# Performance work log

Hardware: AMD Instinct MI355X
Metric: run time of the kernel (lower is better)

## Reference

```python
import jax, jax.numpy as jnp
import numpy as np

B, S, E, H, D, NE, R = 2, 2048, 2048, 16, 128, 8, 16
HALF = D // 2
THETA = 10000.0


def setup_inputs() -> dict:
    key = jax.random.key(0)
    ks = jax.random.split(key, 18)

    def w(k, shape, fan_in):
        return jax.random.normal(k, shape, jnp.float32) / np.float32(np.sqrt(fan_in))

    inp = {
        "x": jax.random.normal(ks[0], (B, S, E), jnp.float32),
        "expert_mask": jax.random.uniform(ks[1], (B, S, NE), dtype=jnp.float32),
    }
    for i, n in enumerate(("q", "k", "v")):
        inp["W" + n] = w(ks[2 + 3 * i], (H * D, E), E)
        inp["b" + n] = jnp.zeros((H * D,), jnp.float32)
        inp["A" + n] = w(ks[3 + 3 * i], (NE, R, E), E)
        inp["B" + n] = w(ks[4 + 3 * i], (H * D, NE, R), R)
    inp["Wo"] = w(ks[11], (E, H * D), H * D)
    inp["bo"] = jnp.zeros((E,), jnp.float32)
    inp["Ao"] = w(ks[12], (NE, R, H * D), H * D)
    inp["Bo"] = w(ks[13], (E, NE, R), R)
    return inp


def routed_linear(x, W, b, A, Bm, mask):
    """MaybeRoutedLinear: dense base + expert-routed low-rank path gated by mask [B,S,NE]."""
    y = jnp.einsum("bsi,oi->bso", x, W) + b
    h = jnp.einsum("bsi,eri->bser", x, A) * mask[..., None]  # [B,S,NE,R]
    return y + jnp.einsum("bser,oer->bso", h, Bm)


def apply_rope(t):
    """Llama-style rotary embedding. t: [B,S,H,D]."""
    inv_freq = 1.0 / (THETA ** (jnp.arange(0, D, 2, dtype=jnp.float32) / D))  # [D/2]
    freqs = jnp.arange(S, dtype=jnp.float32)[:, None] * inv_freq[None, :]  # [S,D/2]
    cos = jnp.concatenate([jnp.cos(freqs)] * 2, -1)[None, :, None, :]  # [1,S,1,D]
    sin = jnp.concatenate([jnp.sin(freqs)] * 2, -1)[None, :, None, :]
    rot = jnp.concatenate([-t[..., HALF:], t[..., :HALF]], -1)
    return t * cos + rot * sin


def reference(x, expert_mask, Wq, bq, Aq, Bq, Wk, bk, Ak, Bk, Wv, bv, Av, Bv, Wo, bo, Ao, Bo):
    q = routed_linear(x, Wq, bq, Aq, Bq, expert_mask).reshape(B, S, H, D)
    k = routed_linear(x, Wk, bk, Ak, Bk, expert_mask).reshape(B, S, H, D)
    v = routed_linear(x, Wv, bv, Av, Bv, expert_mask).reshape(B, S, H, D)
    q = apply_rope(q)
    k = apply_rope(k)
    scores = jnp.einsum("bqhd,bkhd->bhqk", q, k) / jnp.float32(np.sqrt(D))
    causal = jnp.tril(jnp.ones((S, S), dtype=bool))
    scores = jnp.where(causal[None, None], scores, jnp.finfo(scores.dtype).min)
    probs = jax.nn.softmax(scores, axis=-1)
    o = jnp.einsum("bhqk,bkhd->bqhd", probs, v).reshape(B, S, H * D)
    return routed_linear(o, Wo, bo, Ao, Bo, expert_mask)
```

## Files before the change

### kernel.cpp

```cpp
#include <hip/hip_runtime.h>


#define B_ 2
#define S_ 2048
#define E_ 2048
#define H_ 16
#define D_ 128
#define NE_ 8
#define R_ 16
#define HD_ 2048
#define M_ 4096
#define KL_ 128

typedef unsigned short u16;
typedef unsigned int u32;
typedef __attribute__((ext_vector_type(8))) short bf16x8;
typedef __attribute__((ext_vector_type(4))) float f32x4;

typedef const __attribute__((address_space(1))) void gvoid_t;
typedef __attribute__((address_space(3))) void svoid_t;

__device__ __forceinline__ float bf2f(u16 u) {
    union { u32 i; float f; } v; v.i = ((u32)u) << 16; return v.f;
}
__device__ __forceinline__ u16 f2bf(float f) {
    union { float f; u32 i; } v; v.f = f;
    u32 x = v.i;
    return (u16)((x + 0x7fffu + ((x >> 16) & 1u)) >> 16);
}
__device__ __forceinline__ float ldf(const void* p, size_t i, int f) {
    return f ? ((const float*)p)[i] : bf2f(((const u16*)p)[i]);
}
__device__ __forceinline__ float4 ld4(const void* p, size_t i, int f) {
    if (f) return *(const float4*)((const float*)p + i);
    ushort4 v = *(const ushort4*)((const u16*)p + i);
    return make_float4(bf2f(v.x), bf2f(v.y), bf2f(v.z), bf2f(v.w));
}

__global__ void k_detect(const void* __restrict__ x, int* __restrict__ flags) {
    __shared__ int votes[2];
    int tid = threadIdx.x;
    if (tid < 2) votes[tid] = 0;
    __syncthreads();
    const u32* p = (const u32*)x;
    int bad = 0, tot = 0;
    for (int i = tid; i < 4096; i += 64) {
        u32 lo = p[i] & 0xffffu;
        if (lo) {
            tot++;
            int e = (int)((lo >> 7) & 0xffu);
            if (e < 100 || e > 150) bad++;
        }
    }
    atomicAdd(&votes[0], bad);
    atomicAdd(&votes[1], tot);
    __syncthreads();
    if (tid == 0) flags[0] = (votes[1] > 0 && votes[0] * 10 > votes[1] * 3) ? 1 : 0;
}

__global__ void k_cvt(const void* __restrict__ src, u16* __restrict__ dst, int n,
                      const int* __restrict__ flags) {
    int fin = flags[0];
    int i = (blockIdx.x * 256 + threadIdx.x) * 4;
    if (i >= n) return;
    float4 v = ld4(src, i, fin);
    ushort4 o;
    o.x = f2bf(v.x); o.y = f2bf(v.y); o.z = f2bf(v.z); o.w = f2bf(v.w);
    *(ushort4*)(dst + i) = o;
}

#define NX_  8388608L
#define NA1_ 262144L
#define NW_  4194304L
__global__ void k_cvt_all(
    const void* __restrict__ x,
    const void* __restrict__ Aq, const void* __restrict__ Ak,
    const void* __restrict__ Av, const void* __restrict__ Ao,
    const void* __restrict__ Bq, const void* __restrict__ Bk,
    const void* __restrict__ Bv, const void* __restrict__ Bo,
    const void* __restrict__ Wq, const void* __restrict__ Wk,
    const void* __restrict__ Wv,
    u16* __restrict__ Xb, u16* __restrict__ Acat, u16* __restrict__ Bmcat,
    u16* __restrict__ Wcat,
    const int* __restrict__ flags) {
    int fin = flags[0];
    long i = (long)(blockIdx.x * 256 + threadIdx.x) * 4;
    const void* src; u16* dst; long off;
    if (i < NX_) { src = x; dst = Xb; off = i; }
    else if (i < NX_ + 4 * NA1_) {
        long j = i - NX_; int p = (int)(j >> 18); off = j & (NA1_ - 1);
        src = (p == 0) ? Aq : (p == 1) ? Ak : (p == 2) ? Av : Ao;
        dst = Acat + (long)p * NA1_;
    } else if (i < NX_ + 8 * NA1_) {
        long j = i - NX_ - 4 * NA1_; int p = (int)(j >> 18); off = j & (NA1_ - 1);
        src = (p == 0) ? Bq : (p == 1) ? Bk : (p == 2) ? Bv : Bo;
        dst = Bmcat + (long)p * NA1_;
    } else {
        long j = i - NX_ - 8 * NA1_; int p = (int)(j / NW_); off = j - (long)p * NW_;
        src = (p == 0) ? Wq : (p == 1) ? Wk : Wv;
        dst = Wcat + (long)p * NW_;
    }
    float4 v = ld4(src, off, fin);
    ushort4 o;
    o.x = f2bf(v.x); o.y = f2bf(v.y); o.z = f2bf(v.z); o.w = f2bf(v.w);
    *(ushort4*)(dst + off) = o;
}

#define BM_ 128
#define BN_ 128
#define BK_ 64

__global__ __launch_bounds__(256, 2) void k_gemm_mfma(
    const u16* __restrict__ A, int lda,
    const u16* __restrict__ Bw, int ldb, int K1,
    const u16* __restrict__ A2, int lda2,
    const u16* __restrict__ B2, int K2,
    const void* __restrict__ bias, const void* __restrict__ mask,
    void* __restrict__ C, int ldc, int store_mode,
    const int* __restrict__ flags) {
    __shared__ __align__(16) u16 As[BM_ * BK_];
    __shared__ __align__(16) u16 Bs[BN_ * BK_];
    int fin = flags[0];
    int tid = threadIdx.x;
    int w = tid >> 6, lane = tid & 63;
    int l15 = lane & 15, quad = lane >> 4;
    int wm = w >> 1, wn = w & 1;
    int m0 = blockIdx.y * BM_, n0 = blockIdx.x * BN_;
    int lrow = lane >> 3;
    int lcol = (lane & 7) * 8;

    f32x4 acc[4][4];
#pragma unroll
    for (int mt = 0; mt < 4; mt++)
#pragma unroll
        for (int nt = 0; nt < 4; nt++)
#pragma unroll
            for (int r = 0; r < 4; r++) acc[mt][nt][r] = 0.f;

    int n1 = K1 / BK_, n2 = K2 / BK_;
    int total = n1 + n2;
    for (int it = 0; it < total; it++) {
        const u16 *pa, *pb; int sa, sb, kb;
        if (it < n1) { pa = A;  sa = lda;  pb = Bw; sb = ldb; kb = it * BK_; }
        else         { pa = A2; sa = lda2; pb = B2; sb = K2;  kb = (it - n1) * BK_; }
        __syncthreads();
#pragma unroll
        for (int i = 0; i < 4; i++) {
            int rowb = (w * 4 + i) * 8;
            int r = rowb + lrow;
            __builtin_amdgcn_global_load_lds(
                (gvoid_t*)(pa + (size_t)(m0 + r) * sa + kb + lcol),
                (svoid_t*)(As + rowb * BK_), 16, 0, 0);
            __builtin_amdgcn_global_load_lds(
                (gvoid_t*)(pb + (size_t)(n0 + r) * sb + kb + lcol),
                (svoid_t*)(Bs + rowb * BK_), 16, 0, 0);
        }
        __syncthreads();
#pragma unroll
        for (int kk = 0; kk < 2; kk++) {
            int ko = kk * 32 + quad * 8;
            bf16x8 af[4], bf[4];
#pragma unroll
            for (int mt = 0; mt < 4; mt++)
                af[mt] = *(const bf16x8*)(As + (wm * 64 + mt * 16 + l15) * BK_ + ko);
#pragma unroll
            for (int nt = 0; nt < 4; nt++)
                bf[nt] = *(const bf16x8*)(Bs + (wn * 64 + nt * 16 + l15) * BK_ + ko);
#pragma unroll
            for (int mt = 0; mt < 4; mt++)
#pragma unroll
                for (int nt = 0; nt < 4; nt++)
                    acc[mt][nt] = __builtin_amdgcn_mfma_f32_16x16x32_bf16(
                        af[mt], bf[nt], acc[mt][nt], 0, 0, 0);
        }
    }

#pragma unroll
    for (int mt = 0; mt < 4; mt++) {
#pragma unroll
        for (int r = 0; r < 4; r++) {
            int m = m0 + wm * 64 + mt * 16 + quad * 4 + r;
#pragma unroll
            for (int nt = 0; nt < 4; nt++) {
                int n = n0 + wn * 64 + nt * 16 + l15;
                float v = acc[mt][nt][r];
                if (bias) v += ldf(bias, (size_t)n, fin);
                if (mask) v *= ldf(mask, (size_t)m * NE_ + ((n & 127) >> 4), fin);
                int f32out = (store_mode == 2) ? fin : store_mode;
                if (f32out) ((float*)C)[(size_t)m * ldc + n] = v;
                else        ((u16*)C)[(size_t)m * ldc + n] = f2bf(v);
            }
        }
    }
}

#define GBM 256
#define GBN 256
#define GBK 32

__global__ __launch_bounds__(512, 2) void k_gemm256(
    const u16* __restrict__ A, int lda,
    const u16* __restrict__ Bw, int ldb, int K1,
    const u16* __restrict__ A2, int lda2,
    const u16* __restrict__ B2, int K2,
    const void* __restrict__ bias0, const void* __restrict__ bias1,
    const void* __restrict__ bias2,
    void* __restrict__ C, int ldc, int store_mode,
    const int* __restrict__ flags) {
    __shared__ __align__(16) u16 As[4][GBM * GBK];
    __shared__ __align__(16) u16 Bs[4][GBN * GBK];
    int fin = flags[0];
    int tid = threadIdx.x;
    int w = tid >> 6, lane = tid & 63;
    int l15 = lane & 15, quad = lane >> 4;
    int wm = w >> 2, wn = w & 3;

    int nxt = gridDim.x;
    int lin = blockIdx.y * gridDim.x + blockIdx.x;
    int cpx = (gridDim.x * gridDim.y) >> 3;
    int wg = (lin & 7) * cpx + (lin >> 3);
    int m0 = (wg / nxt) * GBM;
    int n0 = (wg % nxt) * GBN;

    int p = (store_mode == 3) ? (n0 >> 11) : 0;
    const u16* A2p = A2 + p * 128;
    const u16* B2p = B2 + (long)p * NA1_;
    int nloc = (store_mode == 3) ? (n0 & 2047) : n0;

    int srow = tid >> 2;
    int scol = (tid & 3) * 8;
    int nk1 = K1 >> 5;
    int NT = nk1 + (K2 >> 5);

    f32x4 acc[8][4];
#pragma unroll
    for (int mt = 0; mt < 8; mt++)
#pragma unroll
        for (int nt = 0; nt < 4; nt++)
#pragma unroll
            for (int r = 0; r < 4; r++) acc[mt][nt][r] = 0.f;

    auto stage = [&](int kt) {
        const u16 *pa, *pb; int sa, sb, kb, nb;
        if (kt < nk1) { pa = A;   sa = lda;  pb = Bw;  sb = ldb; kb = kt * GBK; nb = n0; }
        else          { pa = A2p; sa = lda2; pb = B2p; sb = K2;  kb = (kt - nk1) * GBK; nb = nloc; }
        int buf = kt & 3;
#pragma unroll
        for (int j = 0; j < 2; j++) {
            __builtin_amdgcn_global_load_lds(
                (gvoid_t*)(pa + (size_t)(m0 + j * 128 + srow) * sa + kb + scol),
                (svoid_t*)(&As[buf][(j * 128 + w * 16) * GBK]), 16, 0, 0);
            __builtin_amdgcn_global_load_lds(
                (gvoid_t*)(pb + (size_t)(nb + j * 128 + srow) * sb + kb + scol),
                (svoid_t*)(&Bs[buf][(j * 128 + w * 16) * GBK]), 16, 0, 0);
        }
    };

    stage(0);
    if (NT > 1) stage(1);
    if (NT > 2) stage(2);

    for (int kt = 0; kt < NT; kt++) {
        int buf = kt & 3;
        if (kt + 3 < NT) {
            stage(kt + 3);
            asm volatile("s_waitcnt vmcnt(12)" ::: "memory");
        } else {
            int rem = NT - 1 - kt;
            if (rem >= 2)      asm volatile("s_waitcnt vmcnt(8)" ::: "memory");
            else if (rem == 1) asm volatile("s_waitcnt vmcnt(4)" ::: "memory");
            else               asm volatile("s_waitcnt vmcnt(0)" ::: "memory");
        }
        __builtin_amdgcn_s_barrier();
        __builtin_amdgcn_sched_barrier(0);

        bf16x8 af[8], bfr[4];
#pragma unroll
        for (int mt = 0; mt < 8; mt++)
            af[mt] = *(const bf16x8*)(&As[buf][(wm * 128 + mt * 16 + l15) * GBK + quad * 8]);
#pragma unroll
        for (int nt = 0; nt < 4; nt++)
            bfr[nt] = *(const bf16x8*)(&Bs[buf][(wn * 64 + nt * 16 + l15) * GBK + quad * 8]);

        __builtin_amdgcn_s_setprio(1);
#pragma unroll
        for (int mt = 0; mt < 8; mt++)
#pragma unroll
            for (int nt = 0; nt < 4; nt++)
                acc[mt][nt] = __builtin_amdgcn_mfma_f32_16x16x32_bf16(
                    af[mt], bfr[nt], acc[mt][nt], 0, 0, 0);
        __builtin_amdgcn_s_setprio(0);

        __builtin_amdgcn_s_barrier();
        __builtin_amdgcn_sched_barrier(0);
    }

    const void* bp = (store_mode == 3) ? (p == 0 ? bias0 : p == 1 ? bias1 : bias2)
                                       : bias0;
#pragma unroll
    for (int mt = 0; mt < 8; mt++) {
#pragma unroll
        for (int r = 0; r < 4; r++) {
            int m = m0 + wm * 128 + mt * 16 + quad * 4 + r;
#pragma unroll
            for (int nt = 0; nt < 4; nt++) {
                int n = n0 + wn * 64 + nt * 16 + l15;
                float v = acc[mt][nt][r];
                if (bp) v += ldf(bp, (size_t)(n & 2047), fin);
                if (store_mode == 3) {
                    ((u16*)C)[(size_t)p * 8388608 + (size_t)m * 2048 + (n & 2047)] = f2bf(v);
                } else {
                    if (fin) ((float*)C)[(size_t)m * ldc + n] = v;
                    else     ((u16*)C)[(size_t)m * ldc + n] = f2bf(v);
                }
            }
        }
    }
}

__global__ void k_rope2(u16* __restrict__ Q, u16* __restrict__ K) {
    const int n = M_ * HD_ / 2;
    int idx = blockIdx.x * 256 + threadIdx.x;
    u16* Y = (idx < n) ? Q : K;
    int id = (idx < n) ? idx : idx - n;
    int d2 = id & 63;
    int sh = id >> 6;
    int s = (sh >> 4) & (S_ - 1);
    float inv = powf(10000.f, -(float)d2 * (1.f / 64.f));
    float fr = (float)s * inv;
    float c, sn;
    sincosf(fr, &sn, &c);
    size_t base = ((size_t)sh) << 7;
    float t0 = bf2f(Y[base + d2]);
    float t1 = bf2f(Y[base + d2 + 64]);
    Y[base + d2]      = f2bf(t0 * c - t1 * sn);
    Y[base + d2 + 64] = f2bf(t1 * c + t0 * sn);
}

__global__ void k_transpose_v(const u16* __restrict__ Vb, u16* __restrict__ Vt) {
    __shared__ u16 t[32][33];
    int s0 = blockIdx.x * 32;
    int n0 = blockIdx.y * 32;
    int b  = blockIdx.z;
    int tx = threadIdx.x & 31, ty = threadIdx.x >> 5;
#pragma unroll
    for (int r = 0; r < 4; r++)
        t[ty + r * 8][tx] = Vb[((size_t)(b * S_ + s0 + ty + r * 8)) * HD_ + n0 + tx];
    __syncthreads();
#pragma unroll
    for (int r = 0; r < 4; r++)
        Vt[((size_t)(b * HD_ + n0 + ty + r * 8)) * S_ + s0 + tx] = t[tx][ty + r * 8];
}

#define KS_ST 136
#define VT_ST 72
#define SCALE_ 0.088388347648318447f

__global__ __launch_bounds__(256, 3) void k_flash6(
    const u16* __restrict__ Q, const u16* __restrict__ K,
    const u16* __restrict__ Vt, u16* __restrict__ O) {
    __shared__ __align__(16) u16 Ks[64 * KS_ST];
    __shared__ __align__(16) u16 Vs[128 * VT_ST];
    __shared__ __align__(16) u16 Ps[64 * VT_ST];
    int tid = threadIdx.x;
    int w = tid >> 6, lane = tid & 63;
    int l15 = lane & 15, quad = lane >> 4;
    int bh = blockIdx.y, b = bh >> 4, h = bh & 15;
    int t = 31 - blockIdx.x;
    int q0 = t * 64;

    int krow[4], kd8[4], vd[4], vkg[4];
#pragma unroll
    for (int it = 0; it < 4; it++) {
        int idx = it * 256 + tid;
        krow[it] = idx >> 4; kd8[it] = (idx & 15) * 8;
        vd[it] = idx >> 3;   vkg[it] = (idx & 7) * 8;
    }

    bf16x8 qf[4];
    size_t baseQ = ((size_t)(b * S_ + q0 + w * 16 + l15)) * HD_ + h * D_;
#pragma unroll
    for (int ks = 0; ks < 4; ks++)
        qf[ks] = *(const bf16x8*)(Q + baseQ + ks * 32 + quad * 8);

    f32x4 of[8];
#pragma unroll
    for (int nt = 0; nt < 8; nt++)
#pragma unroll
        for (int r = 0; r < 4; r++) of[nt][r] = 0.f;
    float mreg = -30000.f, lreg = 0.f;
    int qrow = q0 + w * 16 + l15;

    int nch = t + 1;

    bf16x8 kpre[4], vpre[4];
#pragma unroll
    for (int it = 0; it < 4; it++) {
        kpre[it] = *(const bf16x8*)(K + ((size_t)(b * S_ + krow[it])) * HD_ + h * D_ + kd8[it]);
        vpre[it] = *(const bf16x8*)(Vt + ((size_t)(bh * 128 + vd[it])) * S_ + vkg[it]);
    }

    for (int c = 0; c < nch; c++) {
        int k0 = c * 64;
        __syncthreads();
#pragma unroll
        for (int it = 0; it < 4; it++) {
            *(bf16x8*)(Ks + krow[it] * KS_ST + kd8[it]) = kpre[it];
            *(bf16x8*)(Vs + vd[it] * VT_ST + vkg[it]) = vpre[it];
        }
        __syncthreads();
        if (c + 1 < nch) {
            int k1 = k0 + 64;
#pragma unroll
            for (int it = 0; it < 4; it++) {
                kpre[it] = *(const bf16x8*)(K + ((size_t)(b * S_ + k1 + krow[it])) * HD_ + h * D_ + kd8[it]);
                vpre[it] = *(const bf16x8*)(Vt + ((size_t)(bh * 128 + vd[it])) * S_ + k1 + vkg[it]);
            }
        }

        f32x4 sf[4];
#pragma unroll
        for (int nt = 0; nt < 4; nt++)
#pragma unroll
            for (int r = 0; r < 4; r++) sf[nt][r] = 0.f;
#pragma unroll
        for (int ks = 0; ks < 4; ks++) {
            int koff = ks * 32 + quad * 8;
            bf16x8 qa = qf[ks];
#pragma unroll
            for (int nt = 0; nt < 4; nt++) {
                bf16x8 kb = *(const bf16x8*)(Ks + (nt * 16 + l15) * KS_ST + koff);
                sf[nt] = __builtin_amdgcn_mfma_f32_16x16x32_bf16(kb, qa, sf[nt], 0, 0, 0);
            }
        }

#pragma unroll
        for (int nt = 0; nt < 4; nt++) {
            int keyb = k0 + nt * 16 + quad * 4;
#pragma unroll
            for (int r = 0; r < 4; r++) {
                float sv = sf[nt][r] * SCALE_;
                sf[nt][r] = (keyb + r > qrow) ? -30000.f : sv;
            }
        }

        float t0 = fmaxf(fmaxf(sf[0][0], sf[0][1]), fmaxf(sf[0][2], sf[0][3]));
        float t1 = fmaxf(fmaxf(sf[1][0], sf[1][1]), fmaxf(sf[1][2], sf[1][3]));
        float t2 = fmaxf(fmaxf(sf[2][0], sf[2][1]), fmaxf(sf[2][2], sf[2][3]));
        float t3 = fmaxf(fmaxf(sf[3][0], sf[3][1]), fmaxf(sf[3][2], sf[3][3]));
        float cmax = fmaxf(fmaxf(t0, t1), fmaxf(t2, t3));
        cmax = fmaxf(cmax, __shfl_xor(cmax, 16, 64));
        cmax = fmaxf(cmax, __shfl_xor(cmax, 32, 64));
        float mnew = fmaxf(mreg, cmax);
        float a = __expf(mreg - mnew);
        mreg = mnew;
#pragma unroll
        for (int nt = 0; nt < 4; nt++)
#pragma unroll
            for (int r = 0; r < 4; r++)
                sf[nt][r] = __expf(sf[nt][r] - mnew);
        float s0 = (sf[0][0] + sf[0][1]) + (sf[0][2] + sf[0][3]);
        float s1 = (sf[1][0] + sf[1][1]) + (sf[1][2] + sf[1][3]);
        float s2 = (sf[2][0] + sf[2][1]) + (sf[2][2] + sf[2][3]);
        float s3 = (sf[3][0] + sf[3][1]) + (sf[3][2] + sf[3][3]);
        float psum = (s0 + s1) + (s2 + s3);
        psum += __shfl_xor(psum, 16, 64);
        psum += __shfl_xor(psum, 32, 64);
        lreg = lreg * a + psum;

        float al[4];
#pragma unroll
        for (int r = 0; r < 4; r++) al[r] = __shfl(a, quad * 4 + r, 16);

#pragma unroll
        for (int nt = 0; nt < 4; nt++)
#pragma unroll
            for (int r = 0; r < 4; r++)
                Ps[(w * 16 + l15) * VT_ST + nt * 16 + quad * 4 + r] = f2bf(sf[nt][r]);
#pragma unroll
        for (int nt = 0; nt < 8; nt++)
#pragma unroll
            for (int r = 0; r < 4; r++) of[nt][r] *= al[r];

#pragma unroll
        for (int ks2 = 0; ks2 < 2; ks2++) {
            int koff = ks2 * 32 + quad * 8;
            bf16x8 pa = *(const bf16x8*)(Ps + (w * 16 + l15) * VT_ST + koff);
#pragma unroll
            for (int nt = 0; nt < 8; nt++) {
                bf16x8 vb = *(const bf16x8*)(Vs + (nt * 16 + l15) * VT_ST + koff);
                of[nt] = __builtin_amdgcn_mfma_f32_16x16x32_bf16(pa, vb, of[nt], 0, 0, 0);
            }
        }
    }

    float linv = 1.f / lreg;
    float inv[4];
#pragma unroll
    for (int r = 0; r < 4; r++) inv[r] = __shfl(linv, quad * 4 + r, 16);
    int rowb = q0 + w * 16 + quad * 4;
#pragma unroll
    for (int r = 0; r < 4; r++) {
        size_t base = ((size_t)(b * S_ + rowb + r)) * HD_ + h * D_;
#pragma unroll
        for (int nt = 0; nt < 8; nt++)
            O[base + nt * 16 + l15] = f2bf(of[nt][r] * inv[r]);
    }
}

extern "C" void kernel_launch(void* const* d_in, const int* in_sizes, int n_in,
                              void* d_out, int out_size, void* d_ws, size_t ws_size,
                              hipStream_t stream) {
    const void* x    = d_in[0];
    const void* mask = d_in[1];
    const void* Wq = d_in[2];  const void* bq = d_in[3];
    const void* Aq = d_in[4];  const void* Bq = d_in[5];
    const void* Wk = d_in[6];  const void* bk = d_in[7];
    const void* Ak = d_in[8];  const void* Bk = d_in[9];
    const void* Wv = d_in[10]; const void* bv = d_in[11];
    const void* Av = d_in[12]; const void* Bv = d_in[13];
    const void* Wo = d_in[14]; const void* bo = d_in[15];
    const void* Ao = d_in[16]; const void* Bo = d_in[17];

    char* ws = (char*)d_ws;
    const long MB = 1 << 20;
    int* flags = (int*)ws;
    u16* Xb    = (u16*)(ws + 1  * MB);
    u16* Acat  = (u16*)(ws + 17 * MB);
    u16* Bmcat = (u16*)(ws + 19 * MB);
    u16* hg3   = (u16*)(ws + 21 * MB);
    u16* hgo   = (u16*)(ws + 24 * MB);
    u16* Qb    = (u16*)(ws + 25 * MB);
    u16* Kb    = (u16*)(ws + 41 * MB);
    u16* Vb    = (u16*)(ws + 57 * MB);
    u16* Vt    = (u16*)(ws + 73 * MB);
    u16* Wcat  = (u16*)(ws + 73 * MB);
    u16* Wob   = Qb;
    u16* Ob    = Vb;

    k_detect<<<1, 64, 0, stream>>>(x, flags);
    const long NCVT = NX_ + 8 * NA1_ + 3 * NW_;
    k_cvt_all<<<NCVT / 1024, 256, 0, stream>>>(
        x, Aq, Ak, Av, Ao, Bq, Bk, Bv, Bo, Wq, Wk, Wv,
        Xb, Acat, Bmcat, Wcat, flags);

    k_gemm_mfma<<<dim3(3, M_ / BM_), 256, 0, stream>>>(
        Xb, E_, Acat, E_, E_, nullptr, 0, nullptr, 0,
        nullptr, mask, hg3, 384, 0, flags);

    k_gemm256<<<dim3(6144 / GBN, M_ / GBM), 512, 0, stream>>>(
        Xb, E_, Wcat, E_, E_, hg3, 384, Bmcat, KL_,
        bq, bk, bv, Qb, HD_, 3, flags);

    k_rope2<<<(M_ * HD_) / 256, 256, 0, stream>>>(Qb, Kb);
    k_transpose_v<<<dim3(S_ / 32, HD_ / 32, B_), 256, 0, stream>>>(Vb, Vt);

    k_flash6<<<dim3(32, 32), 256, 0, stream>>>(Qb, Kb, Vt, Ob);

    k_cvt<<<NW_ / 1024, 256, 0, stream>>>(Wo, Wob, (int)NW_, flags);
    k_gemm_mfma<<<dim3(1, M_ / BM_), 256, 0, stream>>>(
        Ob, HD_, Acat + 3 * NA1_, E_, E_, nullptr, 0, nullptr, 0,
        nullptr, mask, hgo, KL_, 0, flags);
    k_gemm256<<<dim3(HD_ / GBN, M_ / GBM), 512, 0, stream>>>(
        Ob, HD_, Wob, E_, E_, hgo, KL_, Bmcat + 3 * NA1_, KL_,
        bo, nullptr, nullptr, d_out, HD_, 2, flags);
}
```

Before: 798.5 us.

## Split-K low-rank projection GEMMs and retile main GEMMs with double buffering

The skinny low-rank down-projection GEMMs become split-K kernels across four K slices. They accumulate into zeroed fp32 buffers with atomics, and a separate pass converts the result to bf16, so the small grids fill more of the GPU. The large GEMM becomes a template over N tile width: 256 for the QKV projection and 128 for the output projection, which gives the output GEMM more blocks. It also drops from 4-stage to 2-stage LDS buffering and uses a fragment-major LDS layout. The cost is extra zero and convert launches, atomic traffic, and less prefetch depth, which may expose memory latency.

```diff
diff --git a/kernel.cpp b/kernel.cpp
--- a/kernel.cpp
+++ b/kernel.cpp
@@ -67,6 +67,20 @@
     ushort4 o;
     o.x = f2bf(v.x); o.y = f2bf(v.y); o.z = f2bf(v.z); o.w = f2bf(v.w);
     *(ushort4*)(dst + i) = o;
+}
+
+__global__ void k_cvtf(const float* __restrict__ src, u16* __restrict__ dst, int n) {
+    int i = (blockIdx.x * 256 + threadIdx.x) * 4;
+    if (i >= n) return;
+    float4 v = *(const float4*)(src + i);
+    ushort4 o;
+    o.x = f2bf(v.x); o.y = f2bf(v.y); o.z = f2bf(v.z); o.w = f2bf(v.w);
+    *(ushort4*)(dst + i) = o;
+}
+
+__global__ void k_zero(float4* __restrict__ p, int n4) {
+    int i = blockIdx.x * 256 + threadIdx.x;
+    if (i < n4) p[i] = make_float4(0.f, 0.f, 0.f, 0.f);
 }
 
 #define NX_  8388608L
@@ -110,13 +124,11 @@
 #define BN_ 128
 #define BK_ 64
 
-__global__ __launch_bounds__(256, 2) void k_gemm_mfma(
+__global__ __launch_bounds__(256, 2) void k_gemm_sk(
     const u16* __restrict__ A, int lda,
-    const u16* __restrict__ Bw, int ldb, int K1,
-    const u16* __restrict__ A2, int lda2,
-    const u16* __restrict__ B2, int K2,
-    const void* __restrict__ bias, const void* __restrict__ mask,
-    void* __restrict__ C, int ldc, int store_mode,
+    const u16* __restrict__ Bw, int ldb, int K,
+    const void* __restrict__ mask,
+    float* __restrict__ Cf, int ldc,
     const int* __restrict__ flags) {
     __shared__ __align__(16) u16 As[BM_ * BK_];
     __shared__ __align__(16) u16 Bs[BN_ * BK_];
@@ -137,22 +149,20 @@
 #pragma unroll
             for (int r = 0; r < 4; r++) acc[mt][nt][r] = 0.f;
 
-    int n1 = K1 / BK_, n2 = K2 / BK_;
-    int total = n1 + n2;
-    for (int it = 0; it < total; it++) {
-        const u16 *pa, *pb; int sa, sb, kb;
-        if (it < n1) { pa = A;  sa = lda;  pb = Bw; sb = ldb; kb = it * BK_; }
-        else         { pa = A2; sa = lda2; pb = B2; sb = K2;  kb = (it - n1) * BK_; }
+    int iters = (K / BK_) / gridDim.z;
+    int it0 = blockIdx.z * iters;
+    for (int it = it0; it < it0 + iters; it++) {
+        int kb = it * BK_;
         __syncthreads();
 #pragma unroll
         for (int i = 0; i < 4; i++) {
             int rowb = (w * 4 + i) * 8;
             int r = rowb + lrow;
             __builtin_amdgcn_global_load_lds(
-                (gvoid_t*)(pa + (size_t)(m0 + r) * sa + kb + lcol),
+                (gvoid_t*)(A + (size_t)(m0 + r) * lda + kb + lcol),
                 (svoid_t*)(As + rowb * BK_), 16, 0, 0);
             __builtin_amdgcn_global_load_lds(
-                (gvoid_t*)(pb + (size_t)(n0 + r) * sb + kb + lcol),
+                (gvoid_t*)(Bw + (size_t)(n0 + r) * ldb + kb + lcol),
                 (svoid_t*)(Bs + rowb * BK_), 16, 0, 0);
         }
         __syncthreads();
@@ -183,21 +193,14 @@
 #pragma unroll
             for (int nt = 0; nt < 4; nt++) {
                 int n = n0 + wn * 64 + nt * 16 + l15;
-                float v = acc[mt][nt][r];
-                if (bias) v += ldf(bias, (size_t)n, fin);
-                if (mask) v *= ldf(mask, (size_t)m * NE_ + ((n & 127) >> 4), fin);
-                int f32out = (store_mode == 2) ? fin : store_mode;
-                if (f32out) ((float*)C)[(size_t)m * ldc + n] = v;
-                else        ((u16*)C)[(size_t)m * ldc + n] = f2bf(v);
-            }
-        }
-    }
-}
-
-#define GBM 256
-#define GBN 256
-#define GBK 32
-
+                float v = acc[mt][nt][r] * ldf(mask, (size_t)m * NE_ + ((n & 127) >> 4), fin);
+                atomicAdd(&Cf[(size_t)m * ldc + n], v);
+            }
+        }
+    }
+}
+
+template <int BNt>
 __global__ __launch_bounds__(512, 2) void k_gemm256(
     const u16* __restrict__ A, int lda,
     const u16* __restrict__ Bw, int ldb, int K1,
@@ -207,86 +210,90 @@
     const void* __restrict__ bias2,
     void* __restrict__ C, int ldc, int store_mode,
     const int* __restrict__ flags) {
-    __shared__ __align__(16) u16 As[4][GBM * GBK];
-    __shared__ __align__(16) u16 Bs[4][GBN * GBK];
+    constexpr int NTF = BNt / 64;
+    __shared__ __align__(16) u16 As[2][256 * 32];
+    __shared__ __align__(16) u16 Bs[2][BNt * 32];
     int fin = flags[0];
     int tid = threadIdx.x;
     int w = tid >> 6, lane = tid & 63;
     int l15 = lane & 15, quad = lane >> 4;
     int wm = w >> 2, wn = w & 3;
 
-    int nxt = gridDim.x;
     int lin = blockIdx.y * gridDim.x + blockIdx.x;
     int cpx = (gridDim.x * gridDim.y) >> 3;
     int wg = (lin & 7) * cpx + (lin >> 3);
-    int m0 = (wg / nxt) * GBM;
-    int n0 = (wg % nxt) * GBN;
+    int m0 = (wg / gridDim.x) * 256;
+    int n0 = (wg % gridDim.x) * BNt;
 
     int p = (store_mode == 3) ? (n0 >> 11) : 0;
     const u16* A2p = A2 + p * 128;
     const u16* B2p = B2 + (long)p * NA1_;
     int nloc = (store_mode == 3) ? (n0 & 2047) : n0;
 
-    int srow = tid >> 2;
-    int scol = (tid & 3) * 8;
     int nk1 = K1 >> 5;
     int NT = nk1 + (K2 >> 5);
 
-    f32x4 acc[8][4];
+    f32x4 acc[8][NTF];
 #pragma unroll
     for (int mt = 0; mt < 8; mt++)
 #pragma unroll
-        for (int nt = 0; nt < 4; nt++)
+        for (int nt = 0; nt < NTF; nt++)
 #pragma unroll
             for (int r = 0; r < 4; r++) acc[mt][nt][r] = 0.f;
 
     auto stage = [&](int kt) {
-        const u16 *pa, *pb; int sa, sb, kb, nb;
-        if (kt < nk1) { pa = A;   sa = lda;  pb = Bw;  sb = ldb; kb = kt * GBK; nb = n0; }
-        else          { pa = A2p; sa = lda2; pb = B2p; sb = K2;  kb = (kt - nk1) * GBK; nb = nloc; }
-        int buf = kt & 3;
+        const u16 *pa, *pb; size_t sa, sb; int kb, nb;
+        if (kt < nk1) { pa = A;   sa = lda;  pb = Bw;  sb = ldb; kb = kt * 32; nb = n0; }
+        else          { pa = A2p; sa = lda2; pb = B2p; sb = K2;  kb = (kt - nk1) * 32; nb = nloc; }
+        int buf = kt & 1;
 #pragma unroll
         for (int j = 0; j < 2; j++) {
+            int s = w * 2 + j;
             __builtin_amdgcn_global_load_lds(
-                (gvoid_t*)(pa + (size_t)(m0 + j * 128 + srow) * sa + kb + scol),
-                (svoid_t*)(&As[buf][(j * 128 + w * 16) * GBK]), 16, 0, 0);
+                (gvoid_t*)(pa + (size_t)(m0 + s * 16 + l15) * sa + kb + quad * 8),
+                (svoid_t*)(&As[buf][s * 512]), 16, 0, 0);
+        }
+        if constexpr (BNt == 256) {
+#pragma unroll
+            for (int j = 0; j < 2; j++) {
+                int s = w * 2 + j;
+                __builtin_amdgcn_global_load_lds(
+                    (gvoid_t*)(pb + (size_t)(nb + s * 16 + l15) * sb + kb + quad * 8),
+                    (svoid_t*)(&Bs[buf][s * 512]), 16, 0, 0);
+            }
+        } else {
             __builtin_amdgcn_global_load_lds(
-                (gvoid_t*)(pb + (size_t)(nb + j * 128 + srow) * sb + kb + scol),
-                (svoid_t*)(&Bs[buf][(j * 128 + w * 16) * GBK]), 16, 0, 0);
+                (gvoid_t*)(pb + (size_t)(nb + w * 16 + l15) * sb + kb + quad * 8),
+                (svoid_t*)(&Bs[buf][w * 512]), 16, 0, 0);
         }
     };
 
     stage(0);
-    if (NT > 1) stage(1);
-    if (NT > 2) stage(2);
-
     for (int kt = 0; kt < NT; kt++) {
-        int buf = kt & 3;
-        if (kt + 3 < NT) {
-            stage(kt + 3);
-            asm volatile("s_waitcnt vmcnt(12)" ::: "memory");
+        int buf = kt & 1;
+        if (kt + 1 < NT) {
+            stage(kt + 1);
+            if constexpr (BNt == 256) asm volatile("s_waitcnt vmcnt(4)" ::: "memory");
+            else                      asm volatile("s_waitcnt vmcnt(3)" ::: "memory");
         } else {
-            int rem = NT - 1 - kt;
-            if (rem >= 2)      asm volatile("s_waitcnt vmcnt(8)" ::: "memory");
-            else if (rem == 1) asm volatile("s_waitcnt vmcnt(4)" ::: "memory");
-            else               asm volatile("s_waitcnt vmcnt(0)" ::: "memory");
+            asm volatile("s_waitcnt vmcnt(0)" ::: "memory");
         }
         __builtin_amdgcn_s_barrier();
         __builtin_amdgcn_sched_barrier(0);
 
-        bf16x8 af[8], bfr[4];
+        bf16x8 af[8], bfr[NTF];
 #pragma unroll
         for (int mt = 0; mt < 8; mt++)
-            af[mt] = *(const bf16x8*)(&As[buf][(wm * 128 + mt * 16 + l15) * GBK + quad * 8]);
-#pragma unroll
-        for (int nt = 0; nt < 4; nt++)
-            bfr[nt] = *(const bf16x8*)(&Bs[buf][(wn * 64 + nt * 16 + l15) * GBK + quad * 8]);
+            af[mt] = *(const bf16x8*)(&As[buf][(wm * 8 + mt) * 512 + lane * 8]);
+#pragma unroll
+        for (int nt = 0; nt < NTF; nt++)
+            bfr[nt] = *(const bf16x8*)(&Bs[buf][(wn * NTF + nt) * 512 + lane * 8]);
 
         __builtin_amdgcn_s_setprio(1);
 #pragma unroll
         for (int mt = 0; mt < 8; mt++)
 #pragma unroll
-            for (int nt = 0; nt < 4; nt++)
+            for (int nt = 0; nt < NTF; nt++)
                 acc[mt][nt] = __builtin_amdgcn_mfma_f32_16x16x32_bf16(
                     af[mt], bfr[nt], acc[mt][nt], 0, 0, 0);
         __builtin_amdgcn_s_setprio(0);
@@ -303,8 +310,8 @@
         for (int r = 0; r < 4; r++) {
             int m = m0 + wm * 128 + mt * 16 + quad * 4 + r;
 #pragma unroll
-            for (int nt = 0; nt < 4; nt++) {
-                int n = n0 + wn * 64 + nt * 16 + l15;
+            for (int nt = 0; nt < NTF; nt++) {
+                int n = n0 + wn * (BNt / 4) + nt * 16 + l15;
                 float v = acc[mt][nt][r];
                 if (bp) v += ldf(bp, (size_t)(n & 2047), fin);
                 if (store_mode == 3) {
@@ -535,20 +542,23 @@
     u16* Vb    = (u16*)(ws + 57 * MB);
     u16* Vt    = (u16*)(ws + 73 * MB);
     u16* Wcat  = (u16*)(ws + 73 * MB);
+    float* hg3f = (float*)Qb;
+    float* hgof = (float*)Kb;
     u16* Wob   = Qb;
     u16* Ob    = Vb;
 
     k_detect<<<1, 64, 0, stream>>>(x, flags);
+    k_zero<<<1536, 256, 0, stream>>>((float4*)hg3f, 393216);
     const long NCVT = NX_ + 8 * NA1_ + 3 * NW_;
     k_cvt_all<<<NCVT / 1024, 256, 0, stream>>>(
         x, Aq, Ak, Av, Ao, Bq, Bk, Bv, Bo, Wq, Wk, Wv,
         Xb, Acat, Bmcat, Wcat, flags);
 
-    k_gemm_mfma<<<dim3(3, M_ / BM_), 256, 0, stream>>>(
-        Xb, E_, Acat, E_, E_, nullptr, 0, nullptr, 0,
-        nullptr, mask, hg3, 384, 0, flags);
-
-    k_gemm256<<<dim3(6144 / GBN, M_ / GBM), 512, 0, stream>>>(
+    k_gemm_sk<<<dim3(3, M_ / BM_, 4), 256, 0, stream>>>(
+        Xb, E_, Acat, E_, E_, mask, hg3f, 384, flags);
+    k_cvtf<<<1536, 256, 0, stream>>>(hg3f, hg3, 1572864);
+
+    k_gemm256<256><<<dim3(6144 / 256, M_ / 256), 512, 0, stream>>>(
         Xb, E_, Wcat, E_, E_, hg3, 384, Bmcat, KL_,
         bq, bk, bv, Qb, HD_, 3, flags);
 
@@ -557,11 +567,13 @@
 
     k_flash6<<<dim3(32, 32), 256, 0, stream>>>(Qb, Kb, Vt, Ob);
 
+    k_zero<<<512, 256, 0, stream>>>((float4*)hgof, 131072);
     k_cvt<<<NW_ / 1024, 256, 0, stream>>>(Wo, Wob, (int)NW_, flags);
-    k_gemm_mfma<<<dim3(1, M_ / BM_), 256, 0, stream>>>(
-        Ob, HD_, Acat + 3 * NA1_, E_, E_, nullptr, 0, nullptr, 0,
-        nullptr, mask, hgo, KL_, 0, flags);
-    k_gemm256<<<dim3(HD_ / GBN, M_ / GBM), 512, 0, stream>>>(
+    k_gemm_sk<<<dim3(1, M_ / BM_, 4), 256, 0, stream>>>(
+        Ob, HD_, Acat + 3 * NA1_, E_, E_, mask, hgof, KL_, flags);
+    k_cvtf<<<512, 256, 0, stream>>>(hgof, hgo, 524288);
+
+    k_gemm256<128><<<dim3(HD_ / 128, M_ / 256), 512, 0, stream>>>(
         Ob, HD_, Wob, E_, E_, hgo, KL_, Bmcat + 3 * NA1_, KL_,
         bo, nullptr, nullptr, d_out, HD_, 2, flags);
 }
```

New measurement: 797.5 us. Within noise of the previous version (-0.1%).
